# Kernel tuning notes

Measured on AMD Instinct MI355X. Metric: run time of the kernel, lower is better.

The kernel has to match this reference:

```python
import jax, jax.numpy as jnp
import numpy as np

# mamba-130m-style config (reduced depth for reference harness)
B, L = 4, 512
D_MODEL = 768        # d_model
E = 1536             # d_inner = 2 * d_model
N = 16               # d_state
R = 48               # dt_rank = ceil(d_model/16)
K = 4                # conv kernel
NL = 4               # layers (130m has 24; reduced for harness)
V = 50280            # vocab
H = 1536             # classifier hidden
T = 28               # target_size


def setup_inputs() -> dict:
    key = jax.random.key(0)
    ks = jax.random.split(key, 12)
    def nrm(k, shape, s=0.02):
        return jax.random.normal(k, shape, jnp.float32) * s
    a_log = jnp.tile(jnp.log(jnp.arange(1, N + 1, dtype=jnp.float32))[None, None, :], (NL, E, 1))
    dt_bias = jnp.full((NL, E), float(np.log(np.expm1(0.01))), jnp.float32)
    return {
        "input_ids": jax.random.randint(ks[0], (B, L), 0, V),
        "embed": nrm(ks[1], (V, D_MODEL)),
        "in_proj_w": nrm(ks[2], (NL, D_MODEL, 2 * E)),
        "conv_w": nrm(ks[3], (NL, E, K), 0.2),
        "conv_b": jnp.zeros((NL, E), jnp.float32),
        "x_proj_w": nrm(ks[4], (NL, E, R + 2 * N)),
        "dt_w": nrm(ks[5], (NL, R, E), 0.1),
        "dt_b": dt_bias,
        "A_log": a_log,
        "D_p": jnp.ones((NL, E), jnp.float32),
        "out_w": nrm(ks[6], (NL, E, D_MODEL)),
        "norm_w": jnp.ones((NL, D_MODEL), jnp.float32),
        "norm_f_w": jnp.ones((D_MODEL,), jnp.float32),
        "top_w": nrm(ks[7], (D_MODEL, H)),
        "top_b": jnp.zeros((H,), jnp.float32),
        "bot_w": nrm(ks[8], (H, T)),
        "bot_b": jnp.zeros((T,), jnp.float32),
    }


def rmsnorm(x, w, eps=1e-5):
    return x * jax.lax.rsqrt(jnp.mean(x * x, axis=-1, keepdims=True) + eps) * w


def causal_depthwise_conv(x, w, b):
    # x: (B,L,E), w: (E,K) depthwise causal conv over time
    xt = jnp.transpose(x, (0, 2, 1))  # (B,E,L)
    y = jax.lax.conv_general_dilated(
        xt, w[:, None, :], window_strides=(1,), padding=[(K - 1, 0)],
        dimension_numbers=("NCH", "OIH", "NCH"), feature_group_count=E)
    return jnp.transpose(y + b[None, :, None], (0, 2, 1))


def selective_scan(x, dt, A, Bc, Cc, Dp):
    # x,dt: (B,L,E); A: (E,N); Bc,Cc: (B,L,N); Dp: (E)
    def step(h, inp):
        x_t, dt_t, B_t, C_t = inp  # (B,E),(B,E),(B,N),(B,N)
        dA = jnp.exp(dt_t[..., None] * A)                     # (B,E,N)
        h = dA * h + (dt_t * x_t)[..., None] * B_t[:, None, :]
        y = jnp.einsum("ben,bn->be", h, C_t)
        return h, y
    h0 = jnp.zeros((x.shape[0], E, N), x.dtype)
    xs = (jnp.swapaxes(x, 0, 1), jnp.swapaxes(dt, 0, 1),
          jnp.swapaxes(Bc, 0, 1), jnp.swapaxes(Cc, 0, 1))
    _, ys = jax.lax.scan(step, h0, xs)
    return jnp.swapaxes(ys, 0, 1) + x * Dp


def reference(input_ids, embed, in_proj_w, conv_w, conv_b, x_proj_w, dt_w, dt_b,
              A_log, D_p, out_w, norm_w, norm_f_w, top_w, top_b, bot_w, bot_b):
    h = embed[input_ids]                                      # (B,L,D)
    for i in range(NL):
        xi = rmsnorm(h, norm_w[i])
        xz = xi @ in_proj_w[i]                                # (B,L,2E)
        x, z = xz[..., :E], xz[..., E:]
        x = jax.nn.silu(causal_depthwise_conv(x, conv_w[i], conv_b[i]))
        proj = x @ x_proj_w[i]                                # (B,L,R+2N)
        dt = jax.nn.softplus(proj[..., :R] @ dt_w[i] + dt_b[i])
        Bc, Cc = proj[..., R:R + N], proj[..., R + N:]
        A = -jnp.exp(A_log[i])
        y = selective_scan(x, dt, A, Bc, Cc, D_p[i])
        h = h + (y * jax.nn.silu(z)) @ out_w[i]
    h = rmsnorm(h, norm_f_w)
    cls = h[:, -1, :]                                         # last-token pooling
    # dropout is identity in eval mode
    return jax.nn.relu(cls @ top_w + top_b) @ bot_w + bot_b   # (B,T)
```

## Files before the change

kernel.cpp:

```cpp
#include <hip/hip_runtime.h>
#include <hip/hip_bf16.h>
#include <math.h>

#define B_ 4
#define L_ 512
#define DM 768
#define E_ 1536
#define N_ 16
#define R_ 48
#define K_ 4
#define NL_ 4
#define H_ 1536
#define T_ 28
#define BT_ (B_ * L_)
#define PJ 80

typedef __bf16 bf16x8 __attribute__((ext_vector_type(8)));
typedef float  f32x4  __attribute__((ext_vector_type(4)));

__device__ __forceinline__ float sigmoidf_(float v) { return 1.0f / (1.0f + expf(-v)); }
__device__ __forceinline__ float siluf_(float v) { return v * sigmoidf_(v); }
__device__ __forceinline__ float softplusf_(float v) {
    return fmaxf(v, 0.0f) + log1pf(expf(-fabsf(v)));
}
__device__ __forceinline__ unsigned short f2bf(float x) {
    unsigned u = __float_as_uint(x);
    u = u + 0x7fffu + ((u >> 16) & 1u);
    return (unsigned short)(u >> 16);
}
__device__ __forceinline__ float bf2f(unsigned short h) {
    return __uint_as_float(((unsigned)h) << 16);
}
__device__ __forceinline__ void gl_lds16(const void* g, void* l) {
    auto gp = reinterpret_cast<const __attribute__((address_space(1))) unsigned int*>(
        reinterpret_cast<uintptr_t>(g));
    auto lp = reinterpret_cast<__attribute__((address_space(3))) unsigned int*>(
        reinterpret_cast<uintptr_t>(l));
    __builtin_amdgcn_global_load_lds(gp, lp, 16, 0, 0);
}

__global__ __launch_bounds__(256) void k_embed(const int* __restrict__ ids,
                                               const float* __restrict__ embed,
                                               float* __restrict__ h) {
    int bt = blockIdx.x;
    int tok = ids[bt];
    const float* src = embed + (size_t)tok * DM;
    float* dst = h + (size_t)bt * DM;
    for (int c = threadIdx.x; c < DM; c += 256) dst[c] = src[c];
}

template <bool BF>
__global__ __launch_bounds__(256) void k_rmsnorm(const float* __restrict__ base, long rstride,
                                                 const float* __restrict__ w,
                                                 float* __restrict__ outf,
                                                 unsigned short* __restrict__ oh,
                                                 unsigned short* __restrict__ ol) {
    int tid = threadIdx.x;
    const float* row = base + (size_t)blockIdx.x * rstride;
    float v0 = row[tid], v1 = row[tid + 256], v2 = row[tid + 512];
    float s = v0 * v0 + v1 * v1 + v2 * v2;
#pragma unroll
    for (int m = 1; m < 64; m <<= 1) s += __shfl_xor(s, m);
    __shared__ float red[4];
    if ((tid & 63) == 0) red[tid >> 6] = s;
    __syncthreads();
    s = red[0] + red[1] + red[2] + red[3];
    float rs = rsqrtf(s * (1.0f / (float)DM) + 1e-5f);
    float r0 = v0 * rs * w[tid];
    float r1 = v1 * rs * w[tid + 256];
    float r2 = v2 * rs * w[tid + 512];
    size_t o = (size_t)blockIdx.x * DM;
    if (BF) {
        unsigned short h0 = f2bf(r0), h1 = f2bf(r1), h2 = f2bf(r2);
        oh[o + tid] = h0;        ol[o + tid] = f2bf(r0 - bf2f(h0));
        oh[o + tid + 256] = h1;  ol[o + tid + 256] = f2bf(r1 - bf2f(h1));
        oh[o + tid + 512] = h2;  ol[o + tid + 512] = f2bf(r2 - bf2f(h2));
    } else {
        outf[o + tid] = r0;
        outf[o + tid + 256] = r1;
        outf[o + tid + 512] = r2;
    }
}

__global__ __launch_bounds__(256) void k_wsplit(const float* __restrict__ w,
                                                unsigned short* __restrict__ th,
                                                unsigned short* __restrict__ tl,
                                                int K, int N) {
    __shared__ float t[32][33];
    int n0 = blockIdx.x * 32, k0 = blockIdx.y * 32;
    int c = threadIdx.x & 31, r0 = threadIdx.x >> 5;
#pragma unroll
    for (int it = 0; it < 4; ++it) {
        int r = r0 + it * 8;
        t[r][c] = w[(size_t)(k0 + r) * N + n0 + c];
    }
    __syncthreads();
#pragma unroll
    for (int it = 0; it < 4; ++it) {
        int r = r0 + it * 8;
        float v = t[c][r];
        unsigned short h = f2bf(v);
        th[(size_t)(n0 + r) * K + k0 + c] = h;
        tl[(size_t)(n0 + r) * K + k0 + c] = f2bf(v - bf2f(h));
    }
}

__global__ __launch_bounds__(256) void k_wsplitX(const float* __restrict__ w,
                                                 unsigned short* __restrict__ th,
                                                 unsigned short* __restrict__ tl) {
    __shared__ float t[16][PJ];
    int k0 = blockIdx.x * 16;
    for (int i = threadIdx.x; i < 16 * PJ; i += 256)
        t[i / PJ][i % PJ] = w[(size_t)(k0 + i / PJ) * PJ + i % PJ];
    __syncthreads();
    for (int i = threadIdx.x; i < 16 * PJ; i += 256) {
        int j = i >> 4, kk = i & 15;
        float v = t[kk][j];
        unsigned short h = f2bf(v);
        th[(size_t)j * E_ + k0 + kk] = h;
        tl[(size_t)j * E_ + k0 + kk] = f2bf(v - bf2f(h));
    }
}

template <int BM, int BN, int WR, int WC, bool ACCUM, int KS>
__global__ __launch_bounds__(256) void k_mmf(const unsigned short* __restrict__ Ah,
                                             const unsigned short* __restrict__ Al,
                                             const unsigned short* __restrict__ Bh,
                                             const unsigned short* __restrict__ Bl,
                                             float* __restrict__ C,
                                             int M, int N, int K) {
    constexpr int WM = BM / WR, WN = BN / WC;
    constexpr int MR = WM / 16, NR = WN / 16;
    constexpr int CA = 4 * BM, CB = 4 * BN;
    constexpr int RA = (CA + 255) / 256, RB = (CB + 255) / 256;
    __shared__ __align__(16) unsigned short sAh[CA * 8], sAl[CA * 8];
    __shared__ __align__(16) unsigned short sBh[CB * 8], sBl[CB * 8];
    int tid = threadIdx.x;
    int lane = tid & 63;
    int w = tid >> 6;
    int wr = w / WC, wc = w % WC;
    int m0 = blockIdx.y * BM, n0 = blockIdx.x * BN;
    int kz = (KS > 1) ? blockIdx.z : 0;
    int kb = kz * (K / KS), ke = kb + K / KS;

    f32x4 acc[MR][NR] = {};

    for (int k0 = kb; k0 < ke; k0 += 32) {
#pragma unroll
        for (int r = 0; r < RA; ++r) {
            int cell = (r * 4 + w) * 64 + lane;
            if (CA % 256 == 0 || cell < CA) {
                int oct = cell / BM, row = cell % BM;
                size_t go = (size_t)(m0 + row) * K + k0 + oct * 8;
                gl_lds16(Ah + go, &sAh[(size_t)cell * 8]);
                gl_lds16(Al + go, &sAl[(size_t)cell * 8]);
            }
        }
#pragma unroll
        for (int r = 0; r < RB; ++r) {
            int cell = (r * 4 + w) * 64 + lane;
            if (CB % 256 == 0 || cell < CB) {
                int oct = cell / BN, row = cell % BN;
                size_t go = (size_t)(n0 + row) * K + k0 + oct * 8;
                gl_lds16(Bh + go, &sBh[(size_t)cell * 8]);
                gl_lds16(Bl + go, &sBl[(size_t)cell * 8]);
            }
        }
        asm volatile("s_waitcnt vmcnt(0)" ::: "memory");
        __syncthreads();

        int oct = lane >> 4;
        int rl = lane & 15;
        bf16x8 ah[MR], al[MR], bh[NR], bl[NR];
#pragma unroll
        for (int i = 0; i < MR; ++i) {
            int row = wr * WM + i * 16 + rl;
            ah[i] = *(const bf16x8*)&sAh[(oct * BM + row) * 8];
            al[i] = *(const bf16x8*)&sAl[(oct * BM + row) * 8];
        }
#pragma unroll
        for (int j = 0; j < NR; ++j) {
            int row = wc * WN + j * 16 + rl;
            bh[j] = *(const bf16x8*)&sBh[(oct * BN + row) * 8];
            bl[j] = *(const bf16x8*)&sBl[(oct * BN + row) * 8];
        }
#pragma unroll
        for (int i = 0; i < MR; ++i)
#pragma unroll
            for (int j = 0; j < NR; ++j) {
                acc[i][j] = __builtin_amdgcn_mfma_f32_16x16x32_bf16(ah[i], bh[j], acc[i][j], 0, 0, 0);
                acc[i][j] = __builtin_amdgcn_mfma_f32_16x16x32_bf16(ah[i], bl[j], acc[i][j], 0, 0, 0);
                acc[i][j] = __builtin_amdgcn_mfma_f32_16x16x32_bf16(al[i], bh[j], acc[i][j], 0, 0, 0);
            }
        __syncthreads();
    }
    float* Cw = C + (size_t)kz * M * N;
    int rl = lane & 15, rq = lane >> 4;
#pragma unroll
    for (int i = 0; i < MR; ++i)
#pragma unroll
        for (int j = 0; j < NR; ++j)
#pragma unroll
            for (int v = 0; v < 4; ++v) {
                int row = m0 + wr * WM + i * 16 + rq * 4 + v;
                int col = n0 + wc * WN + j * 16 + rl;
                float val = acc[i][j][v];
                if (ACCUM) val += Cw[(size_t)row * N + col];
                Cw[(size_t)row * N + col] = val;
            }
}

__global__ __launch_bounds__(256) void k_padd(const float* __restrict__ pp,
                                              float* __restrict__ proj) {
    int idx = blockIdx.x * 256 + threadIdx.x;
    const int MN = BT_ * PJ;
    if (idx < MN)
        proj[idx] = pp[idx] + pp[MN + idx] + pp[2 * MN + idx] + pp[3 * MN + idx];
}

__global__ __launch_bounds__(256) void k_conv(const float* __restrict__ xz,
                                              const float* __restrict__ cw,
                                              const float* __restrict__ cb,
                                              float* __restrict__ xc,
                                              unsigned short* __restrict__ xch,
                                              unsigned short* __restrict__ xcl) {
    int idx = blockIdx.x * 256 + threadIdx.x;
    int e = idx % E_;
    int bt = idx / E_;
    int t = bt & (L_ - 1);
    const float* base = xz + (size_t)bt * (2 * E_) + e;
    float w0 = cw[e * 4 + 0], w1 = cw[e * 4 + 1], w2 = cw[e * 4 + 2], w3 = cw[e * 4 + 3];
    float acc = cb[e] + base[0] * w3;
    if (t >= 1) acc += base[-(2 * E_)] * w2;
    if (t >= 2) acc += base[-(4 * E_)] * w1;
    if (t >= 3) acc += base[-(6 * E_)] * w0;
    float v = siluf_(acc);
    xc[idx] = v;
    unsigned short hh = f2bf(v);
    xch[idx] = hh;
    xcl[idx] = f2bf(v - bf2f(hh));
}

__global__ __launch_bounds__(256) void k_prep(const float* __restrict__ proj,
                                              const float* __restrict__ dw,
                                              const float* __restrict__ db,
                                              const float* __restrict__ xc,
                                              const float* __restrict__ xz,
                                              const float* __restrict__ dp,
                                              float* __restrict__ dtT,
                                              float* __restrict__ dxT,
                                              float* __restrict__ xdT,
                                              float* __restrict__ zsT) {
    __shared__ float projS[64][48];
    __shared__ float dwS[48][64];
    __shared__ float tileT[64][65];
    int b = blockIdx.z;
    int t0 = blockIdx.x * 64;
    int e0 = blockIdx.y * 64;
    int tid = threadIdx.x;

    for (int idx = tid; idx < 64 * 48; idx += 256) {
        int tl = idx / 48, k = idx % 48;
        projS[tl][k] = proj[(size_t)(b * L_ + t0 + tl) * PJ + k];
    }
    for (int idx = tid; idx < 48 * 64; idx += 256) {
        int k = idx >> 6, ee = idx & 63;
        dwS[k][ee] = dw[(size_t)k * E_ + e0 + ee];
    }
    __syncthreads();

    int el = tid & 63;
    int tg = tid >> 6;
    float acc[16];
    float bvE = db[e0 + el];
#pragma unroll
    for (int s = 0; s < 16; ++s) acc[s] = bvE;
    for (int k = 0; k < 48; ++k) {
        float wv = dwS[k][el];
#pragma unroll
        for (int s = 0; s < 16; ++s) acc[s] += projS[tg * 16 + s][k] * wv;
    }
    float dtv[16];
#pragma unroll
    for (int s = 0; s < 16; ++s) dtv[s] = softplusf_(acc[s]);
    float xv[16];
#pragma unroll
    for (int s = 0; s < 16; ++s)
        xv[s] = xc[(size_t)(b * L_ + t0 + tg * 16 + s) * E_ + e0 + el];
    float dpv = dp[e0 + el];

#define XPOSE_OUT(dst, EXPR)                                                      \
    do {                                                                          \
        __syncthreads();                                                          \
        for (int s = 0; s < 16; ++s) tileT[el][tg * 16 + s] = (EXPR);             \
        __syncthreads();                                                          \
        for (int idx = tid; idx < 4096; idx += 256) {                             \
            int e2 = idx >> 6, t2 = idx & 63;                                     \
            dst[((size_t)b * E_ + e0 + e2) * L_ + t0 + t2] = tileT[e2][t2];       \
        }                                                                         \
    } while (0)

    XPOSE_OUT(dtT, dtv[s]);
    XPOSE_OUT(dxT, dtv[s] * xv[s]);
    XPOSE_OUT(xdT, xv[s] * dpv);
    float zv[16];
#pragma unroll
    for (int s = 0; s < 16; ++s)
        zv[s] = xz[(size_t)(b * L_ + t0 + tg * 16 + s) * (2 * E_) + E_ + e0 + el];
    XPOSE_OUT(zsT, siluf_(zv[s]));
#undef XPOSE_OUT
}

__global__ __launch_bounds__(256) void k_scan3(const float* __restrict__ dtT,
                                               const float* dxT,
                                               const float* __restrict__ xdT,
                                               const float* __restrict__ zsT,
                                               const float* __restrict__ proj,
                                               const float* __restrict__ A_log,
                                               float* yzT) {
    __shared__ float s_p[16 * 16 * 20];
    __shared__ float sAP[16][17], sAS[16][17], sH[16][17];
    int tid = threadIdx.x;
    int b = blockIdx.x / E_;
    int e = blockIdx.x - b * E_;
    size_t base = ((size_t)b * E_ + e) * L_;

    int c = tid >> 4;
    int n = tid & 15;
    float A = -expf(A_log[e * N_ + n]);

    int t0 = c * 32;
    const float* pdt = dtT + base + t0;
    const float* pdx = dxT + base + t0;
    const float* pb = proj + (size_t)(b * L_ + t0) * PJ + R_ + n;
    const float* pc = pb + N_;

    float dAr[32], ur[32];
    float P = 1.0f, S = 0.0f;
#pragma unroll
    for (int s = 0; s < 32; ++s) {
        float dA = expf(pdt[s] * A);
        float u = pdx[s] * pb[s * PJ];
        dAr[s] = dA;
        ur[s] = u;
        P *= dA;
        S = dA * S + u;
    }
    sAP[c][n] = P;
    sAS[c][n] = S;
    __syncthreads();
    if (tid < 16) {
        float Hc = 0.0f;
        for (int c2 = 0; c2 < 16; ++c2) {
            sH[c2][tid] = Hc;
            Hc = sAP[c2][tid] * Hc + sAS[c2][tid];
        }
    }
    __syncthreads();

    float h = sH[c][n];
    float* myrow = &s_p[(c * 16) * 20 + n];
#pragma unroll
    for (int s = 0; s < 16; ++s) {
        h = dAr[s] * h + ur[s];
        myrow[s * 20] = h * pc[s * PJ];
    }
    __syncthreads();
    {
        int rc = tid >> 4, rs = tid & 15;
        const float* row = &s_p[(rc * 16 + rs) * 20];
        f32x4 v0 = *(const f32x4*)&row[0];
        f32x4 v1 = *(const f32x4*)&row[4];
        f32x4 v2 = *(const f32x4*)&row[8];
        f32x4 v3 = *(const f32x4*)&row[12];
        float sum = (v0[0]+v0[1]+v0[2]+v0[3]) + (v1[0]+v1[1]+v1[2]+v1[3]) +
                    (v2[0]+v2[1]+v2[2]+v2[3]) + (v3[0]+v3[1]+v3[2]+v3[3]);
        int t = rc * 32 + rs;
        yzT[base + t] = (sum + xdT[base + t]) * zsT[base + t];
    }
    __syncthreads();
#pragma unroll
    for (int s = 0; s < 16; ++s) {
        h = dAr[16 + s] * h + ur[16 + s];
        myrow[s * 20] = h * pc[(16 + s) * PJ];
    }
    __syncthreads();
    {
        int rc = tid >> 4, rs = tid & 15;
        const float* row = &s_p[(rc * 16 + rs) * 20];
        f32x4 v0 = *(const f32x4*)&row[0];
        f32x4 v1 = *(const f32x4*)&row[4];
        f32x4 v2 = *(const f32x4*)&row[8];
        f32x4 v3 = *(const f32x4*)&row[12];
        float sum = (v0[0]+v0[1]+v0[2]+v0[3]) + (v1[0]+v1[1]+v1[2]+v1[3]) +
                    (v2[0]+v2[1]+v2[2]+v2[3]) + (v3[0]+v3[1]+v3[2]+v3[3]);
        int t = rc * 32 + 16 + rs;
        yzT[base + t] = (sum + xdT[base + t]) * zsT[base + t];
    }
}

__global__ __launch_bounds__(256) void k_ytr(const float* __restrict__ yzT,
                                             unsigned short* __restrict__ yzh,
                                             unsigned short* __restrict__ yzl) {
    __shared__ float t[64][65];
    int b = blockIdx.z;
    int t0 = blockIdx.x * 64;
    int e0 = blockIdx.y * 64;
    int tid = threadIdx.x;
    for (int idx = tid; idx < 4096; idx += 256) {
        int e2 = idx >> 6, t2 = idx & 63;
        t[e2][t2] = yzT[((size_t)b * E_ + e0 + e2) * L_ + t0 + t2];
    }
    __syncthreads();
    for (int idx = tid; idx < 4096; idx += 256) {
        int t2 = idx >> 6, e2 = idx & 63;
        float v = t[e2][t2];
        unsigned short hh = f2bf(v);
        size_t o = (size_t)(b * L_ + t0 + t2) * E_ + e0 + e2;
        yzh[o] = hh;
        yzl[o] = f2bf(v - bf2f(hh));
    }
}

__global__ __launch_bounds__(256) void k_top(const float* __restrict__ cls,
                                             const float* __restrict__ w,
                                             const float* __restrict__ bias,
                                             float* __restrict__ hrel) {
    __shared__ float xs[B_][DM];
    __shared__ float red[4][64][B_];
    int tid = threadIdx.x;
    for (int c = tid; c < B_ * DM; c += 256) ((float*)xs)[c] = cls[c];
    __syncthreads();
    int jl = tid & 63;
    int kq = tid >> 6;
    int j = blockIdx.x * 64 + jl;
    float acc[B_] = {};
    for (int k = kq * (DM / 4); k < (kq + 1) * (DM / 4); ++k) {
        float wv = w[(size_t)k * H_ + j];
#pragma unroll
        for (int b = 0; b < B_; ++b) acc[b] += xs[b][k] * wv;
    }
#pragma unroll
    for (int b = 0; b < B_; ++b) red[kq][jl][b] = acc[b];
    __syncthreads();
    if (kq == 0) {
        float bv = bias[j];
#pragma unroll
        for (int b = 0; b < B_; ++b) {
            float s = red[0][jl][b] + red[1][jl][b] + red[2][jl][b] + red[3][jl][b] + bv;
            hrel[(size_t)b * H_ + j] = fmaxf(s, 0.0f);
        }
    }
}

__global__ __launch_bounds__(256) void k_bot(const float* __restrict__ hrel,
                                             const float* __restrict__ w,
                                             const float* __restrict__ bias,
                                             float* __restrict__ out) {
    __shared__ float red[8][T_];
    int b = blockIdx.x;
    int jl = threadIdx.x & 31;
    int kq = threadIdx.x >> 5;
    if (jl < T_) {
        float acc = 0.0f;
        for (int k = kq * (H_ / 8); k < (kq + 1) * (H_ / 8); ++k)
            acc += hrel[(size_t)b * H_ + k] * w[(size_t)k * T_ + jl];
        red[kq][jl] = acc;
    }
    __syncthreads();
    if (kq == 0 && jl < T_) {
        float s = bias[jl];
#pragma unroll
        for (int q = 0; q < 8; ++q) s += red[q][jl];
        out[(size_t)b * T_ + jl] = s;
    }
}

extern "C" void kernel_launch(void* const* d_in, const int* in_sizes, int n_in,
                              void* d_out, int out_size, void* d_ws, size_t ws_size,
                              hipStream_t stream) {
    const int*   ids       = (const int*)d_in[0];
    const float* embed     = (const float*)d_in[1];
    const float* in_proj_w = (const float*)d_in[2];
    const float* conv_w    = (const float*)d_in[3];
    const float* conv_b    = (const float*)d_in[4];
    const float* x_proj_w  = (const float*)d_in[5];
    const float* dt_w      = (const float*)d_in[6];
    const float* dt_b      = (const float*)d_in[7];
    const float* A_log     = (const float*)d_in[8];
    const float* D_p       = (const float*)d_in[9];
    const float* out_w     = (const float*)d_in[10];
    const float* norm_w    = (const float*)d_in[11];
    const float* norm_f_w  = (const float*)d_in[12];
    const float* top_w     = (const float*)d_in[13];
    const float* top_b     = (const float*)d_in[14];
    const float* bot_w     = (const float*)d_in[15];
    const float* bot_b     = (const float*)d_in[16];
    float* out = (float*)d_out;

    float* ws = (float*)d_ws;
    float* h    = ws;
    float* xz   = h + (size_t)BT_ * DM;
    float* xc   = xz + (size_t)BT_ * 2 * E_;
    float* proj = xc + (size_t)BT_ * E_;
    float* dtT  = proj + (size_t)BT_ * PJ;
    float* dxT  = dtT + (size_t)BT_ * E_;
    float* xdT  = dxT + (size_t)BT_ * E_;
    float* zsT  = xdT + (size_t)BT_ * E_;
    float* cls  = zsT + (size_t)BT_ * E_;
    float* hrel = cls + (size_t)B_ * DM;
    unsigned short* us = (unsigned short*)(hrel + (size_t)B_ * H_);
    unsigned short* xi_h = us;
    unsigned short* xi_l = xi_h + (size_t)BT_ * DM;
    unsigned short* yz_h = xi_l + (size_t)BT_ * DM;
    unsigned short* yz_l = yz_h + (size_t)BT_ * E_;
    unsigned short* wA_h = yz_l + (size_t)BT_ * E_;
    unsigned short* wA_l = wA_h + (size_t)(2 * E_) * DM;
    unsigned short* wB_h = wA_l + (size_t)(2 * E_) * DM;
    unsigned short* wB_l = wB_h + (size_t)DM * E_;
    unsigned short* xc_h = wB_l + (size_t)DM * E_;
    unsigned short* xc_l = xc_h + (size_t)BT_ * E_;
    unsigned short* wX_h = xc_l + (size_t)BT_ * E_;
    unsigned short* wX_l = wX_h + (size_t)PJ * E_;
    float* pp = (float*)(wX_l + (size_t)PJ * E_);
    float* yzT = dxT;

    k_embed<<<BT_, 256, 0, stream>>>(ids, embed, h);

    for (int i = 0; i < NL_; ++i) {
        const float* ipw = in_proj_w + (size_t)i * DM * 2 * E_;
        const float* cwi = conv_w + (size_t)i * E_ * K_;
        const float* cbi = conv_b + (size_t)i * E_;
        const float* xpw = x_proj_w + (size_t)i * E_ * PJ;
        const float* dwi = dt_w + (size_t)i * R_ * E_;
        const float* dbi = dt_b + (size_t)i * E_;
        const float* ali = A_log + (size_t)i * E_ * N_;
        const float* dpi = D_p + (size_t)i * E_;
        const float* owi = out_w + (size_t)i * E_ * DM;
        const float* nwi = norm_w + (size_t)i * DM;

        k_rmsnorm<true><<<BT_, 256, 0, stream>>>(h, DM, nwi, nullptr, xi_h, xi_l);
        k_wsplit<<<dim3(2 * E_ / 32, DM / 32), 256, 0, stream>>>(ipw, wA_h, wA_l, DM, 2 * E_);
        k_mmf<128, 128, 2, 2, false, 1><<<dim3(2 * E_ / 128, BT_ / 128), 256, 0, stream>>>(
            xi_h, xi_l, wA_h, wA_l, xz, BT_, 2 * E_, DM);
        k_conv<<<BT_ * E_ / 256, 256, 0, stream>>>(xz, cwi, cbi, xc, xc_h, xc_l);
        k_wsplitX<<<E_ / 16, 256, 0, stream>>>(xpw, wX_h, wX_l);
        k_mmf<128, PJ, 4, 1, false, 4><<<dim3(1, BT_ / 128, 4), 256, 0, stream>>>(
            xc_h, xc_l, wX_h, wX_l, pp, BT_, PJ, E_);
        k_padd<<<(BT_ * PJ + 255) / 256, 256, 0, stream>>>(pp, proj);
        k_prep<<<dim3(L_ / 64, E_ / 64, B_), 256, 0, stream>>>(
            proj, dwi, dbi, xc, xz, dpi, dtT, dxT, xdT, zsT);
        k_scan3<<<B_ * E_, 256, 0, stream>>>(dtT, dxT, xdT, zsT, proj, ali, yzT);
        k_ytr<<<dim3(L_ / 64, E_ / 64, B_), 256, 0, stream>>>(yzT, yz_h, yz_l);
        k_wsplit<<<dim3(DM / 32, E_ / 32), 256, 0, stream>>>(owi, wB_h, wB_l, E_, DM);
        k_mmf<64, 64, 2, 2, true, 1><<<dim3(DM / 64, BT_ / 64), 256, 0, stream>>>(
            yz_h, yz_l, wB_h, wB_l, h, BT_, DM, E_);
    }

    k_rmsnorm<false><<<B_, 256, 0, stream>>>(h + (size_t)(L_ - 1) * DM, (long)L_ * DM,
                                             norm_f_w, cls, nullptr, nullptr);
    k_top<<<H_ / 64, 256, 0, stream>>>(cls, top_w, top_b, hrel);
    k_bot<<<B_, 256, 0, stream>>>(hrel, bot_w, bot_b, out);
}
```

Before: 1.283 ms.

## Batch weight splits across layers, drop fp32 conv output, use fast exp

```diff
diff --git a/kernel.cpp b/kernel.cpp
--- a/kernel.cpp
+++ b/kernel.cpp
@@ -18,10 +18,10 @@
 typedef __bf16 bf16x8 __attribute__((ext_vector_type(8)));
 typedef float  f32x4  __attribute__((ext_vector_type(4)));
 
-__device__ __forceinline__ float sigmoidf_(float v) { return 1.0f / (1.0f + expf(-v)); }
+__device__ __forceinline__ float sigmoidf_(float v) { return 1.0f / (1.0f + __expf(-v)); }
 __device__ __forceinline__ float siluf_(float v) { return v * sigmoidf_(v); }
 __device__ __forceinline__ float softplusf_(float v) {
-    return fmaxf(v, 0.0f) + log1pf(expf(-fabsf(v)));
+    return fmaxf(v, 0.0f) + __logf(1.0f + __expf(-fabsf(v)));
 }
 __device__ __forceinline__ unsigned short f2bf(float x) {
     unsigned u = __float_as_uint(x);
@@ -87,12 +87,16 @@
                                                 unsigned short* __restrict__ tl,
                                                 int K, int N) {
     __shared__ float t[32][33];
+    size_t off = (size_t)blockIdx.z * K * N;
+    const float* wz = w + off;
+    unsigned short* thz = th + off;
+    unsigned short* tlz = tl + off;
     int n0 = blockIdx.x * 32, k0 = blockIdx.y * 32;
     int c = threadIdx.x & 31, r0 = threadIdx.x >> 5;
 #pragma unroll
     for (int it = 0; it < 4; ++it) {
         int r = r0 + it * 8;
-        t[r][c] = w[(size_t)(k0 + r) * N + n0 + c];
+        t[r][c] = wz[(size_t)(k0 + r) * N + n0 + c];
     }
     __syncthreads();
 #pragma unroll
@@ -100,8 +104,8 @@
         int r = r0 + it * 8;
         float v = t[c][r];
         unsigned short h = f2bf(v);
-        th[(size_t)(n0 + r) * K + k0 + c] = h;
-        tl[(size_t)(n0 + r) * K + k0 + c] = f2bf(v - bf2f(h));
+        thz[(size_t)(n0 + r) * K + k0 + c] = h;
+        tlz[(size_t)(n0 + r) * K + k0 + c] = f2bf(v - bf2f(h));
     }
 }
 
@@ -109,16 +113,20 @@
                                                  unsigned short* __restrict__ th,
                                                  unsigned short* __restrict__ tl) {
     __shared__ float t[16][PJ];
+    size_t off = (size_t)blockIdx.z * E_ * PJ;
+    const float* wz = w + off;
+    unsigned short* thz = th + off;
+    unsigned short* tlz = tl + off;
     int k0 = blockIdx.x * 16;
     for (int i = threadIdx.x; i < 16 * PJ; i += 256)
-        t[i / PJ][i % PJ] = w[(size_t)(k0 + i / PJ) * PJ + i % PJ];
+        t[i / PJ][i % PJ] = wz[(size_t)(k0 + i / PJ) * PJ + i % PJ];
     __syncthreads();
     for (int i = threadIdx.x; i < 16 * PJ; i += 256) {
         int j = i >> 4, kk = i & 15;
         float v = t[kk][j];
         unsigned short h = f2bf(v);
-        th[(size_t)j * E_ + k0 + kk] = h;
-        tl[(size_t)j * E_ + k0 + kk] = f2bf(v - bf2f(h));
+        thz[(size_t)j * E_ + k0 + kk] = h;
+        tlz[(size_t)j * E_ + k0 + kk] = f2bf(v - bf2f(h));
     }
 }
 
@@ -221,7 +229,6 @@
 __global__ __launch_bounds__(256) void k_conv(const float* __restrict__ xz,
                                               const float* __restrict__ cw,
                                               const float* __restrict__ cb,
-                                              float* __restrict__ xc,
                                               unsigned short* __restrict__ xch,
                                               unsigned short* __restrict__ xcl) {
     int idx = blockIdx.x * 256 + threadIdx.x;
@@ -235,7 +242,6 @@
     if (t >= 2) acc += base[-(4 * E_)] * w1;
     if (t >= 3) acc += base[-(6 * E_)] * w0;
     float v = siluf_(acc);
-    xc[idx] = v;
     unsigned short hh = f2bf(v);
     xch[idx] = hh;
     xcl[idx] = f2bf(v - bf2f(hh));
@@ -244,7 +250,8 @@
 __global__ __launch_bounds__(256) void k_prep(const float* __restrict__ proj,
                                               const float* __restrict__ dw,
                                               const float* __restrict__ db,
-                                              const float* __restrict__ xc,
+                                              const unsigned short* __restrict__ xch,
+                                              const unsigned short* __restrict__ xcl,
                                               const float* __restrict__ xz,
                                               const float* __restrict__ dp,
                                               float* __restrict__ dtT,
@@ -285,8 +292,10 @@
     for (int s = 0; s < 16; ++s) dtv[s] = softplusf_(acc[s]);
     float xv[16];
 #pragma unroll
-    for (int s = 0; s < 16; ++s)
-        xv[s] = xc[(size_t)(b * L_ + t0 + tg * 16 + s) * E_ + e0 + el];
+    for (int s = 0; s < 16; ++s) {
+        size_t ii = (size_t)(b * L_ + t0 + tg * 16 + s) * E_ + e0 + el;
+        xv[s] = bf2f(xch[ii]) + bf2f(xcl[ii]);
+    }
     float dpv = dp[e0 + el];
 
 #define XPOSE_OUT(dst, EXPR)                                                      \
@@ -327,7 +336,7 @@
 
     int c = tid >> 4;
     int n = tid & 15;
-    float A = -expf(A_log[e * N_ + n]);
+    float A = -__expf(A_log[e * N_ + n]);
 
     int t0 = c * 32;
     const float* pdt = dtT + base + t0;
@@ -339,7 +348,7 @@
     float P = 1.0f, S = 0.0f;
 #pragma unroll
     for (int s = 0; s < 32; ++s) {
-        float dA = expf(pdt[s] * A);
+        float dA = __expf(pdt[s] * A);
         float u = pdx[s] * pb[s * PJ];
         dAr[s] = dA;
         ur[s] = u;
@@ -501,8 +510,7 @@
     float* ws = (float*)d_ws;
     float* h    = ws;
     float* xz   = h + (size_t)BT_ * DM;
-    float* xc   = xz + (size_t)BT_ * 2 * E_;
-    float* proj = xc + (size_t)BT_ * E_;
+    float* proj = xz + (size_t)BT_ * 2 * E_;
     float* dtT  = proj + (size_t)BT_ * PJ;
     float* dxT  = dtT + (size_t)BT_ * E_;
     float* xdT  = dxT + (size_t)BT_ * E_;
@@ -514,47 +522,52 @@
     unsigned short* xi_l = xi_h + (size_t)BT_ * DM;
     unsigned short* yz_h = xi_l + (size_t)BT_ * DM;
     unsigned short* yz_l = yz_h + (size_t)BT_ * E_;
-    unsigned short* wA_h = yz_l + (size_t)BT_ * E_;
-    unsigned short* wA_l = wA_h + (size_t)(2 * E_) * DM;
-    unsigned short* wB_h = wA_l + (size_t)(2 * E_) * DM;
-    unsigned short* wB_l = wB_h + (size_t)DM * E_;
-    unsigned short* xc_h = wB_l + (size_t)DM * E_;
+    unsigned short* xc_h = yz_l + (size_t)BT_ * E_;
     unsigned short* xc_l = xc_h + (size_t)BT_ * E_;
-    unsigned short* wX_h = xc_l + (size_t)BT_ * E_;
-    unsigned short* wX_l = wX_h + (size_t)PJ * E_;
-    float* pp = (float*)(wX_l + (size_t)PJ * E_);
+    unsigned short* wA_h = xc_l + (size_t)BT_ * E_;
+    unsigned short* wA_l = wA_h + (size_t)NL_ * 2 * E_ * DM;
+    unsigned short* wB_h = wA_l + (size_t)NL_ * 2 * E_ * DM;
+    unsigned short* wB_l = wB_h + (size_t)NL_ * DM * E_;
+    unsigned short* wX_h = wB_l + (size_t)NL_ * DM * E_;
+    unsigned short* wX_l = wX_h + (size_t)NL_ * PJ * E_;
+    float* pp  = (float*)(wX_l + (size_t)NL_ * PJ * E_);
     float* yzT = dxT;
 
     k_embed<<<BT_, 256, 0, stream>>>(ids, embed, h);
+    k_wsplit<<<dim3(2 * E_ / 32, DM / 32, NL_), 256, 0, stream>>>(
+        in_proj_w, wA_h, wA_l, DM, 2 * E_);
+    k_wsplit<<<dim3(DM / 32, E_ / 32, NL_), 256, 0, stream>>>(
+        out_w, wB_h, wB_l, E_, DM);
+    k_wsplitX<<<dim3(E_ / 16, 1, NL_), 256, 0, stream>>>(x_proj_w, wX_h, wX_l);
 
     for (int i = 0; i < NL_; ++i) {
-        const float* ipw = in_proj_w + (size_t)i * DM * 2 * E_;
         const float* cwi = conv_w + (size_t)i * E_ * K_;
         const float* cbi = conv_b + (size_t)i * E_;
-        const float* xpw = x_proj_w + (size_t)i * E_ * PJ;
         const float* dwi = dt_w + (size_t)i * R_ * E_;
         const float* dbi = dt_b + (size_t)i * E_;
         const float* ali = A_log + (size_t)i * E_ * N_;
         const float* dpi = D_p + (size_t)i * E_;
-        const float* owi = out_w + (size_t)i * E_ * DM;
         const float* nwi = norm_w + (size_t)i * DM;
+        unsigned short* wAh = wA_h + (size_t)i * 2 * E_ * DM;
+        unsigned short* wAl = wA_l + (size_t)i * 2 * E_ * DM;
+        unsigned short* wBh = wB_h + (size_t)i * DM * E_;
+        unsigned short* wBl = wB_l + (size_t)i * DM * E_;
+        unsigned short* wXh = wX_h + (size_t)i * PJ * E_;
+        unsigned short* wXl = wX_l + (size_t)i * PJ * E_;
 
         k_rmsnorm<true><<<BT_, 256, 0, stream>>>(h, DM, nwi, nullptr, xi_h, xi_l);
-        k_wsplit<<<dim3(2 * E_ / 32, DM / 32), 256, 0, stream>>>(ipw, wA_h, wA_l, DM, 2 * E_);
         k_mmf<128, 128, 2, 2, false, 1><<<dim3(2 * E_ / 128, BT_ / 128), 256, 0, stream>>>(
-            xi_h, xi_l, wA_h, wA_l, xz, BT_, 2 * E_, DM);
-        k_conv<<<BT_ * E_ / 256, 256, 0, stream>>>(xz, cwi, cbi, xc, xc_h, xc_l);
-        k_wsplitX<<<E_ / 16, 256, 0, stream>>>(xpw, wX_h, wX_l);
+            xi_h, xi_l, wAh, wAl, xz, BT_, 2 * E_, DM);
+        k_conv<<<BT_ * E_ / 256, 256, 0, stream>>>(xz, cwi, cbi, xc_h, xc_l);
         k_mmf<128, PJ, 4, 1, false, 4><<<dim3(1, BT_ / 128, 4), 256, 0, stream>>>(
-            xc_h, xc_l, wX_h, wX_l, pp, BT_, PJ, E_);
+            xc_h, xc_l, wXh, wXl, pp, BT_, PJ, E_);
         k_padd<<<(BT_ * PJ + 255) / 256, 256, 0, stream>>>(pp, proj);
         k_prep<<<dim3(L_ / 64, E_ / 64, B_), 256, 0, stream>>>(
-            proj, dwi, dbi, xc, xz, dpi, dtT, dxT, xdT, zsT);
+            proj, dwi, dbi, xc_h, xc_l, xz, dpi, dtT, dxT, xdT, zsT);
         k_scan3<<<B_ * E_, 256, 0, stream>>>(dtT, dxT, xdT, zsT, proj, ali, yzT);
         k_ytr<<<dim3(L_ / 64, E_ / 64, B_), 256, 0, stream>>>(yzT, yz_h, yz_l);
-        k_wsplit<<<dim3(DM / 32, E_ / 32), 256, 0, stream>>>(owi, wB_h, wB_l, E_, DM);
         k_mmf<64, 64, 2, 2, true, 1><<<dim3(DM / 64, BT_ / 64), 256, 0, stream>>>(
-            yz_h, yz_l, wB_h, wB_l, h, BT_, DM, E_);
+            yz_h, yz_l, wBh, wBl, h, BT_, DM, E_);
     }
 
     k_rmsnorm<false><<<B_, 256, 0, stream>>>(h + (size_t)(L_ - 1) * DM, (long)L_ * DM,
```

Result: faster. 1.208 ms (-5.8%).
